# Kernel optimization log

Measured on AMD Instinct MI355X. Metric: run time of the kernel, lower is better.

The kernel has to match this reference:

```python
import jax, jax.numpy as jnp
import numpy as np

TOP_K = 2
NUM_EXPERTS = 64
LOAD_BALANCE_ALPHA = 0.01
Z_LOSS_ALPHA = 1e-4
TEMPERATURE = 1.0  # buffer init, clamped to [0.1, 2.0] -> 1.0 (seq_len < 8192 branch)


def setup_inputs() -> dict:
    key = jax.random.key(0)
    k1, k2 = jax.random.split(key)
    x = jax.random.normal(k1, (4, 4096, 1024), dtype=jnp.float32)
    gate_w = jax.random.normal(k2, (NUM_EXPERTS, 1024), dtype=jnp.float32) * (1.0 / np.sqrt(1024))
    return {"x": x, "gate_w": gate_w}


def reference(x, gate_w):
    B, S, H = x.shape
    x_flat = x.reshape(-1, H)                      # [T, H], T = B*S
    logits = jnp.einsum('th,eh->te', x_flat, gate_w)  # [T, E]
    logits = logits / TEMPERATURE
    scores = jax.nn.softmax(logits, axis=-1)       # [T, E]
    # eval path: dynamic_top_k == top_k, no noise / capacity limitation
    top_scores, top_idx = jax.lax.top_k(scores, TOP_K)   # [T, K]
    top_scores = jax.nn.softmax(top_scores.astype(jnp.float32), axis=-1).astype(x.dtype)
    # load-balance loss: squared deviation of mean expert load from uniform
    expert_load = scores.mean(axis=0)              # [E]
    ideal = 1.0 / NUM_EXPERTS
    lb_loss = LOAD_BALANCE_ALPHA * NUM_EXPERTS * jnp.sum((expert_load - ideal) ** 2)
    # z-loss: mean squared logsumexp of gate logits
    z = jax.nn.logsumexp(logits, axis=-1)          # [T]
    z_loss = Z_LOSS_ALPHA * jnp.mean(z ** 2)
    total_loss = lb_loss + z_loss
    return top_scores, top_idx, total_loss
```

## Files before the change

### kernel.cpp

```cpp
#include <hip/hip_runtime.h>
#include <math.h>

#define T_TOK 16384
#define NEXP  64


__global__ void moe_prep(const float* __restrict__ gw, float* __restrict__ ws) {
    __shared__ float tile[64][65];
    const int b = blockIdx.x;
    const int tid = threadIdx.x;
    if (b == 0 && tid < 128) ws[tid] = 0.f;
#pragma unroll
    for (int it = 0; it < 16; ++it) {
        int idx = it * 256 + tid;
        int e = idx >> 6, kk = idx & 63;
        tile[e][kk] = gw[e * 1024 + b * 64 + kk];
    }
    __syncthreads();
#pragma unroll
    for (int it = 0; it < 16; ++it) {
        int idx = it * 256 + tid;
        int kk = idx >> 6, e = idx & 63;
        ws[128 + (b * 64 + kk) * 64 + e] = tile[e][kk];
    }
}

__launch_bounds__(1024, 4)
__global__ void moe_main(const float* __restrict__ x,
                         const float* __restrict__ wt,
                         float* __restrict__ acc_ws,
                         float* __restrict__ out) {
    __shared__ float xbuf[2][4096];
    __shared__ float sc[64][65];
    __shared__ float row_inv[64];
    __shared__ float colpart[16][64];
    __shared__ int   is_last;

    const int tid  = threadIdx.x;
    const int lane = tid & 63;
    const int wv   = tid >> 6;
    const int g     = __builtin_amdgcn_readfirstlane(wv & 3);
    const int h     = __builtin_amdgcn_readfirstlane(wv >> 2);
    const int khalf = __builtin_amdgcn_readfirstlane(h >> 1);
    const int cq    = __builtin_amdgcn_readfirstlane(h & 1);
    const int tok0 = blockIdx.x << 6;

    const int rr = tid >> 4;
    const int cg = tid & 15;
    const float* gbase = x + (((size_t)(tok0 + rr)) << 10) + (cg << 2);
    const int lo = (rr << 6) + ((cg ^ (rr & 15)) << 2);
    float* xb = &xbuf[0][0];

    float acc[16];
#pragma unroll
    for (int e = 0; e < 16; ++e) acc[e] = 0.f;

    float4 p0 = *(const float4*)(gbase);
    float4 p1 = *(const float4*)(gbase + 512);

    const int swz = lane & 15;
    const float* xrow = &xbuf[khalf][lane << 6];

#pragma unroll 1
    for (int s = 0; s < 8; ++s) {
        __syncthreads();
        *(float4*)(xb + lo)        = p0;
        *(float4*)(xb + lo + 4096) = p1;
        __syncthreads();
        if (s < 7) {
            const float* gs = gbase + ((s + 1) << 6);
            p0 = *(const float4*)(gs);
            p1 = *(const float4*)(gs + 512);
        }
        const float* wrow = wt + (((khalf << 9) + (s << 6)) << 6) + (g << 4);
#pragma unroll
        for (int c = 0; c < 8; ++c) {
            int cc = (cq << 3) + c;
            float4 xv = *(const float4*)(xrow + ((cc ^ swz) << 2));
            float xa[4] = {xv.x, xv.y, xv.z, xv.w};
#pragma unroll
            for (int j = 0; j < 4; ++j) {
                const float* wkj = wrow + (((cc << 2) + j) << 6);
                float xj = xa[j];
#pragma unroll
                for (int e = 0; e < 16; ++e)
                    acc[e] = fmaf(xj, wkj[e], acc[e]);
            }
        }
    }

    if (h == 0) {
#pragma unroll
        for (int e = 0; e < 16; ++e) sc[lane][(g << 4) + e] = acc[e];
    }
    __syncthreads();
    if (h == 1) {
#pragma unroll
        for (int e = 0; e < 16; ++e) sc[lane][(g << 4) + e] += acc[e];
    }
    __syncthreads();
    if (h == 2) {
#pragma unroll
        for (int e = 0; e < 16; ++e) sc[lane][(g << 4) + e] += acc[e];
    }
    __syncthreads();
    if (h == 3) {
#pragma unroll
        for (int e = 0; e < 16; ++e) sc[lane][(g << 4) + e] += acc[e];
    }
    __syncthreads();

    if (tid < 64) {
        const int r = tid;
        float v1 = -1e30f, v2 = -1e30f;
        int i1 = 0, i2 = 0;
        for (int j = 0; j < 64; ++j) {
            float l = sc[r][j];
            if (l > v1)      { v2 = v1; i2 = i1; v1 = l; i1 = j; }
            else if (l > v2) { v2 = l; i2 = j; }
        }
        float m = v1;
        float ssum = 0.f;
        for (int j = 0; j < 64; ++j) {
            float ev = expf(sc[r][j] - m);
            ssum += ev;
            sc[r][j] = ev;
        }
        float inv = 1.f / ssum;
        row_inv[r] = inv;
        float z = m + logf(ssum);
        float zsq = z * z;
#pragma unroll
        for (int off = 32; off > 0; off >>= 1) zsq += __shfl_down(zsq, off);
        if (lane == 0) atomicAdd(acc_ws + 64, zsq);

        float p1s = inv;
        float p2s = expf(v2 - m) * inv;
        float bb  = expf(p2s - p1s);
        float s1 = 1.f / (1.f + bb);
        float s2 = bb * s1;
        int t = tok0 + r;
        out[2 * t]     = s1;
        out[2 * t + 1] = s2;
        out[2 * T_TOK + 2 * t]     = (float)i1;
        out[2 * T_TOK + 2 * t + 1] = (float)i2;
    }
    __syncthreads();

    {
        int e  = tid & 63;
        int rg = tid >> 6;
        float sum = 0.f;
#pragma unroll
        for (int r2 = 0; r2 < 4; ++r2) {
            int row = (rg << 2) + r2;
            sum += sc[row][e] * row_inv[row];
        }
        colpart[rg][e] = sum;
    }
    __syncthreads();
    if (tid < 64) {
        float tot = 0.f;
#pragma unroll
        for (int rg = 0; rg < 16; ++rg) tot += colpart[rg][tid];
        atomicAdd(acc_ws + tid, tot);
    }

    __syncthreads();
    if (tid == 0) {
        __threadfence();
        int old = __hip_atomic_fetch_add((int*)(acc_ws + 66), 1,
                                         __ATOMIC_ACQ_REL, __HIP_MEMORY_SCOPE_AGENT);
        is_last = (old == 255) ? 1 : 0;
    }
    __syncthreads();
    if (is_last && tid < 64) {
        __threadfence();
        float load = __hip_atomic_load(acc_ws + tid, __ATOMIC_RELAXED,
                                       __HIP_MEMORY_SCOPE_AGENT) * (1.f / 16384.f);
        float d = load - (1.f / 64.f);
        float v = d * d;
#pragma unroll
        for (int off = 32; off > 0; off >>= 1) v += __shfl_down(v, off);
        if (tid == 0) {
            float zsum = __hip_atomic_load(acc_ws + 64, __ATOMIC_RELAXED,
                                           __HIP_MEMORY_SCOPE_AGENT);
            float lb = 0.01f * 64.f * v;
            float zl = 1e-4f * zsum * (1.f / 16384.f);
            out[4 * T_TOK] = lb + zl;
        }
    }
}

extern "C" void kernel_launch(void* const* d_in, const int* in_sizes, int n_in,
                              void* d_out, int out_size, void* d_ws, size_t ws_size,
                              hipStream_t stream) {
    const float* x  = (const float*)d_in[0];
    const float* gw = (const float*)d_in[1];
    float* out = (float*)d_out;
    float* ws  = (float*)d_ws;

    moe_prep<<<16, 256, 0, stream>>>(gw, ws);
    moe_main<<<256, 1024, 0, stream>>>(x, ws + 128, ws, out);
}
```

Before: 134.8 us.

## Stage gate weights in LDS and use 4x4 register tiles for logits

The inner GEMV loop now stages both an x tile and a weight tile in shared memory for each 64-wide K chunk. Each thread computes a 4-token by 4-expert register tile instead of one token against 16 experts read straight from global memory. This is meant to cut redundant global and L1 reads of the transposed weights and raise the FMA-to-load ratio through outer-product reuse. In exchange it runs twice as many pipeline stages and barriers (16 instead of 8), and the logit buffer is repadded to a row stride of 68 so the partial sums can be stored as float4.

```diff
diff --git a/kernel.cpp b/kernel.cpp
--- a/kernel.cpp
+++ b/kernel.cpp
@@ -30,8 +30,9 @@
                          const float* __restrict__ wt,
                          float* __restrict__ acc_ws,
                          float* __restrict__ out) {
-    __shared__ float xbuf[2][4096];
-    __shared__ float sc[64][65];
+    __shared__ float xbuf[4096];
+    __shared__ float wbuf[4096];
+    __shared__ float sc[64 * 68];
     __shared__ float row_inv[64];
     __shared__ float colpart[16][64];
     __shared__ int   is_last;
@@ -39,92 +40,136 @@
     const int tid  = threadIdx.x;
     const int lane = tid & 63;
     const int wv   = tid >> 6;
-    const int g     = __builtin_amdgcn_readfirstlane(wv & 3);
-    const int h     = __builtin_amdgcn_readfirstlane(wv >> 2);
-    const int khalf = __builtin_amdgcn_readfirstlane(h >> 1);
-    const int cq    = __builtin_amdgcn_readfirstlane(h & 1);
+    const int kq   = __builtin_amdgcn_readfirstlane(wv & 3);
+    const int tile = __builtin_amdgcn_readfirstlane(wv >> 2);
+    const int tt = tile >> 1, te = tile & 1;
+    const int ta = lane >> 3;
+    const int eb = lane & 7;
     const int tok0 = blockIdx.x << 6;
 
     const int rr = tid >> 4;
     const int cg = tid & 15;
-    const float* gbase = x + (((size_t)(tok0 + rr)) << 10) + (cg << 2);
-    const int lo = (rr << 6) + ((cg ^ (rr & 15)) << 2);
-    float* xb = &xbuf[0][0];
+    const float* gx = x + (((size_t)(tok0 + rr)) << 10) + ((cg >> 2) << 8) + ((cg & 3) << 2);
+    const int xlo = (rr << 6) + ((cg ^ (rr & 15)) << 2);
+    const float* gw = wt + ((((rr >> 4) << 8) + (rr & 15)) << 6) + (cg << 2);
+    const int wlo = (rr << 6) + (cg << 2);
 
     float acc[16];
 #pragma unroll
     for (int e = 0; e < 16; ++e) acc[e] = 0.f;
 
-    float4 p0 = *(const float4*)(gbase);
-    float4 p1 = *(const float4*)(gbase + 512);
-
-    const int swz = lane & 15;
-    const float* xrow = &xbuf[khalf][lane << 6];
+    const int t0 = (tt << 5) + (ta << 2);
+    const float* xrow0 = xbuf + ((t0 + 0) << 6);
+    const float* xrow1 = xbuf + ((t0 + 1) << 6);
+    const float* xrow2 = xbuf + ((t0 + 2) << 6);
+    const float* xrow3 = xbuf + ((t0 + 3) << 6);
+    const int c0 = (t0 + 0) & 15, c1 = (t0 + 1) & 15;
+    const int c2 = (t0 + 2) & 15, c3 = (t0 + 3) & 15;
+    const int ebase = (te << 5) + (eb << 2);
+    const float* wp = wbuf + (kq << 10) + ebase;
+    const int cwb = kq << 2;
+
+    float4 px = *(const float4*)gx;
+    float4 pw = *(const float4*)gw;
 
 #pragma unroll 1
-    for (int s = 0; s < 8; ++s) {
+    for (int s = 0; s < 16; ++s) {
         __syncthreads();
-        *(float4*)(xb + lo)        = p0;
-        *(float4*)(xb + lo + 4096) = p1;
+        *(float4*)(xbuf + xlo) = px;
+        *(float4*)(wbuf + wlo) = pw;
         __syncthreads();
-        if (s < 7) {
-            const float* gs = gbase + ((s + 1) << 6);
-            p0 = *(const float4*)(gs);
-            p1 = *(const float4*)(gs + 512);
-        }
-        const float* wrow = wt + (((khalf << 9) + (s << 6)) << 6) + (g << 4);
-#pragma unroll
-        for (int c = 0; c < 8; ++c) {
-            int cc = (cq << 3) + c;
-            float4 xv = *(const float4*)(xrow + ((cc ^ swz) << 2));
-            float xa[4] = {xv.x, xv.y, xv.z, xv.w};
-#pragma unroll
-            for (int j = 0; j < 4; ++j) {
-                const float* wkj = wrow + (((cc << 2) + j) << 6);
-                float xj = xa[j];
-#pragma unroll
-                for (int e = 0; e < 16; ++e)
-                    acc[e] = fmaf(xj, wkj[e], acc[e]);
-            }
-        }
-    }
-
-    if (h == 0) {
-#pragma unroll
-        for (int e = 0; e < 16; ++e) sc[lane][(g << 4) + e] = acc[e];
-    }
-    __syncthreads();
-    if (h == 1) {
-#pragma unroll
-        for (int e = 0; e < 16; ++e) sc[lane][(g << 4) + e] += acc[e];
-    }
-    __syncthreads();
-    if (h == 2) {
-#pragma unroll
-        for (int e = 0; e < 16; ++e) sc[lane][(g << 4) + e] += acc[e];
-    }
-    __syncthreads();
-    if (h == 3) {
-#pragma unroll
-        for (int e = 0; e < 16; ++e) sc[lane][(g << 4) + e] += acc[e];
+        if (s < 15) {
+            px = *(const float4*)(gx + ((s + 1) << 4));
+            pw = *(const float4*)(gw + ((s + 1) << 10));
+        }
+#pragma unroll
+        for (int g4 = 0; g4 < 4; ++g4) {
+            const int cw = cwb + g4;
+            float4 xf0 = *(const float4*)(xrow0 + ((cw ^ c0) << 2));
+            float4 xf1 = *(const float4*)(xrow1 + ((cw ^ c1) << 2));
+            float4 xf2 = *(const float4*)(xrow2 + ((cw ^ c2) << 2));
+            float4 xf3 = *(const float4*)(xrow3 + ((cw ^ c3) << 2));
+            const float* wq = wp + (g4 << 8);
+            float4 wf0 = *(const float4*)(wq);
+            float4 wf1 = *(const float4*)(wq + 64);
+            float4 wf2 = *(const float4*)(wq + 128);
+            float4 wf3 = *(const float4*)(wq + 192);
+            float xa[16] = {xf0.x, xf0.y, xf0.z, xf0.w,
+                            xf1.x, xf1.y, xf1.z, xf1.w,
+                            xf2.x, xf2.y, xf2.z, xf2.w,
+                            xf3.x, xf3.y, xf3.z, xf3.w};
+            float wa[16] = {wf0.x, wf0.y, wf0.z, wf0.w,
+                            wf1.x, wf1.y, wf1.z, wf1.w,
+                            wf2.x, wf2.y, wf2.z, wf2.w,
+                            wf3.x, wf3.y, wf3.z, wf3.w};
+#pragma unroll
+            for (int i = 0; i < 4; ++i)
+#pragma unroll
+                for (int u = 0; u < 4; ++u) {
+                    float xv = xa[(i << 2) + u];
+#pragma unroll
+                    for (int j = 0; j < 4; ++j)
+                        acc[(i << 2) + j] = fmaf(xv, wa[(u << 2) + j], acc[(i << 2) + j]);
+                }
+        }
+    }
+
+    if (kq == 0) {
+#pragma unroll
+        for (int i = 0; i < 4; ++i) {
+            float4 v = make_float4(acc[(i << 2)], acc[(i << 2) + 1],
+                                   acc[(i << 2) + 2], acc[(i << 2) + 3]);
+            *(float4*)(sc + (t0 + i) * 68 + ebase) = v;
+        }
+    }
+    __syncthreads();
+    if (kq == 1) {
+#pragma unroll
+        for (int i = 0; i < 4; ++i) {
+            float4 o = *(float4*)(sc + (t0 + i) * 68 + ebase);
+            o.x += acc[(i << 2)];     o.y += acc[(i << 2) + 1];
+            o.z += acc[(i << 2) + 2]; o.w += acc[(i << 2) + 3];
+            *(float4*)(sc + (t0 + i) * 68 + ebase) = o;
+        }
+    }
+    __syncthreads();
+    if (kq == 2) {
+#pragma unroll
+        for (int i = 0; i < 4; ++i) {
+            float4 o = *(float4*)(sc + (t0 + i) * 68 + ebase);
+            o.x += acc[(i << 2)];     o.y += acc[(i << 2) + 1];
+            o.z += acc[(i << 2) + 2]; o.w += acc[(i << 2) + 3];
+            *(float4*)(sc + (t0 + i) * 68 + ebase) = o;
+        }
+    }
+    __syncthreads();
+    if (kq == 3) {
+#pragma unroll
+        for (int i = 0; i < 4; ++i) {
+            float4 o = *(float4*)(sc + (t0 + i) * 68 + ebase);
+            o.x += acc[(i << 2)];     o.y += acc[(i << 2) + 1];
+            o.z += acc[(i << 2) + 2]; o.w += acc[(i << 2) + 3];
+            *(float4*)(sc + (t0 + i) * 68 + ebase) = o;
+        }
     }
     __syncthreads();
 
     if (tid < 64) {
         const int r = tid;
+        const float* srow = sc + r * 68;
         float v1 = -1e30f, v2 = -1e30f;
         int i1 = 0, i2 = 0;
         for (int j = 0; j < 64; ++j) {
-            float l = sc[r][j];
+            float l = srow[j];
             if (l > v1)      { v2 = v1; i2 = i1; v1 = l; i1 = j; }
             else if (l > v2) { v2 = l; i2 = j; }
         }
         float m = v1;
         float ssum = 0.f;
         for (int j = 0; j < 64; ++j) {
-            float ev = expf(sc[r][j] - m);
+            float ev = expf(srow[j] - m);
             ssum += ev;
-            sc[r][j] = ev;
+            sc[r * 68 + j] = ev;
         }
         float inv = 1.f / ssum;
         row_inv[r] = inv;
@@ -154,7 +199,7 @@
 #pragma unroll
         for (int r2 = 0; r2 < 4; ++r2) {
             int row = (rg << 2) + r2;
-            sum += sc[row][e] * row_inv[row];
+            sum += sc[row * 68 + e] * row_inv[row];
         }
         colpart[rg][e] = sum;
     }
```

Result: faster. 130.6 us (-3.1%).

## Stage gate weights in LDS and use 8x8 register-tiled outer-product GEMM

Applied to the files above, without the earlier changes.

Replaces the pre-transposed global weight read with per-block LDS staging of both x and gate_w tiles (padded stride 68). Each thread now computes an 8-token by 8-expert outer-product tile with 64 accumulators, and the 16 waves split the K dimension. The separate transpose kernel is dropped for a trivial zeroing kernel. The cost is a longer serialized cross-wave reduction through LDS in eight sync-separated rounds, plus higher register pressure under the 1024-thread launch bound.

```diff
diff --git a/kernel.cpp b/kernel.cpp
--- a/kernel.cpp
+++ b/kernel.cpp
@@ -3,35 +3,32 @@
 
 #define T_TOK 16384
 #define NEXP  64
-
-
-__global__ void moe_prep(const float* __restrict__ gw, float* __restrict__ ws) {
-    __shared__ float tile[64][65];
-    const int b = blockIdx.x;
-    const int tid = threadIdx.x;
-    if (b == 0 && tid < 128) ws[tid] = 0.f;
-#pragma unroll
-    for (int it = 0; it < 16; ++it) {
-        int idx = it * 256 + tid;
-        int e = idx >> 6, kk = idx & 63;
-        tile[e][kk] = gw[e * 1024 + b * 64 + kk];
-    }
-    __syncthreads();
-#pragma unroll
-    for (int it = 0; it < 16; ++it) {
-        int idx = it * 256 + tid;
-        int kk = idx >> 6, e = idx & 63;
-        ws[128 + (b * 64 + kk) * 64 + e] = tile[e][kk];
-    }
+#define STR   68
+
+
+__global__ void moe_zero(float* __restrict__ ws) {
+    if (threadIdx.x < 128) ws[threadIdx.x] = 0.f;
 }
+
+#define FMA_ROW(i, xv) do {                                                    \
+    acc[((i) << 3) + 0] = fmaf((xv), wf0.x, acc[((i) << 3) + 0]);              \
+    acc[((i) << 3) + 1] = fmaf((xv), wf0.y, acc[((i) << 3) + 1]);              \
+    acc[((i) << 3) + 2] = fmaf((xv), wf0.z, acc[((i) << 3) + 2]);              \
+    acc[((i) << 3) + 3] = fmaf((xv), wf0.w, acc[((i) << 3) + 3]);              \
+    acc[((i) << 3) + 4] = fmaf((xv), wf1.x, acc[((i) << 3) + 4]);              \
+    acc[((i) << 3) + 5] = fmaf((xv), wf1.y, acc[((i) << 3) + 5]);              \
+    acc[((i) << 3) + 6] = fmaf((xv), wf1.z, acc[((i) << 3) + 6]);              \
+    acc[((i) << 3) + 7] = fmaf((xv), wf1.w, acc[((i) << 3) + 7]);              \
+} while (0)
 
 __launch_bounds__(1024, 4)
 __global__ void moe_main(const float* __restrict__ x,
-                         const float* __restrict__ wt,
+                         const float* __restrict__ gw,
                          float* __restrict__ acc_ws,
                          float* __restrict__ out) {
-    __shared__ float xbuf[2][4096];
-    __shared__ float sc[64][65];
+    __shared__ __align__(16) float xbuf[64 * STR];
+    __shared__ __align__(16) float wbuf[64 * STR];
+    __shared__ __align__(16) float sc[64 * STR];
     __shared__ float row_inv[64];
     __shared__ float colpart[16][64];
     __shared__ int   is_last;
@@ -39,92 +36,125 @@
     const int tid  = threadIdx.x;
     const int lane = tid & 63;
     const int wv   = tid >> 6;
-    const int g     = __builtin_amdgcn_readfirstlane(wv & 3);
-    const int h     = __builtin_amdgcn_readfirstlane(wv >> 2);
-    const int khalf = __builtin_amdgcn_readfirstlane(h >> 1);
-    const int cq    = __builtin_amdgcn_readfirstlane(h & 1);
+    const int kbase = __builtin_amdgcn_readfirstlane(wv << 2);
+    const int tq = lane >> 3;
+    const int eq = lane & 7;
     const int tok0 = blockIdx.x << 6;
 
-    const int rr = tid >> 4;
-    const int cg = tid & 15;
-    const float* gbase = x + (((size_t)(tok0 + rr)) << 10) + (cg << 2);
-    const int lo = (rr << 6) + ((cg ^ (rr & 15)) << 2);
-    float* xb = &xbuf[0][0];
-
-    float acc[16];
-#pragma unroll
-    for (int e = 0; e < 16; ++e) acc[e] = 0.f;
-
-    float4 p0 = *(const float4*)(gbase);
-    float4 p1 = *(const float4*)(gbase + 512);
-
-    const int swz = lane & 15;
-    const float* xrow = &xbuf[khalf][lane << 6];
+    const int srow = tid >> 4;
+    const int kc   = tid & 15;
+    const float* gx = x  + ((size_t)(tok0 + srow) << 10) + kc;
+    const float* gwp = gw + ((size_t)srow << 10) + kc;
+    const int slo = kc * STR + srow;
+
+    float acc[64];
+#pragma unroll
+    for (int i = 0; i < 64; ++i) acc[i] = 0.f;
+
+    float px0 = gx[0],  px1 = gx[16],  px2 = gx[32],  px3 = gx[48];
+    float pw0 = gwp[0], pw1 = gwp[16], pw2 = gwp[32], pw3 = gwp[48];
+
+    const float* xr = xbuf + kbase * STR + (tq << 3);
+    const float* wr = wbuf + kbase * STR + (eq << 3);
 
 #pragma unroll 1
-    for (int s = 0; s < 8; ++s) {
+    for (int s = 0; s < 16; ++s) {
         __syncthreads();
-        *(float4*)(xb + lo)        = p0;
-        *(float4*)(xb + lo + 4096) = p1;
+        xbuf[slo]            = px0;
+        xbuf[slo + 16 * STR] = px1;
+        xbuf[slo + 32 * STR] = px2;
+        xbuf[slo + 48 * STR] = px3;
+        wbuf[slo]            = pw0;
+        wbuf[slo + 16 * STR] = pw1;
+        wbuf[slo + 32 * STR] = pw2;
+        wbuf[slo + 48 * STR] = pw3;
         __syncthreads();
-        if (s < 7) {
-            const float* gs = gbase + ((s + 1) << 6);
-            p0 = *(const float4*)(gs);
-            p1 = *(const float4*)(gs + 512);
-        }
-        const float* wrow = wt + (((khalf << 9) + (s << 6)) << 6) + (g << 4);
-#pragma unroll
-        for (int c = 0; c < 8; ++c) {
-            int cc = (cq << 3) + c;
-            float4 xv = *(const float4*)(xrow + ((cc ^ swz) << 2));
-            float xa[4] = {xv.x, xv.y, xv.z, xv.w};
-#pragma unroll
-            for (int j = 0; j < 4; ++j) {
-                const float* wkj = wrow + (((cc << 2) + j) << 6);
-                float xj = xa[j];
-#pragma unroll
-                for (int e = 0; e < 16; ++e)
-                    acc[e] = fmaf(xj, wkj[e], acc[e]);
+        if (s < 15) {
+            const float* g2 = gx  + ((s + 1) << 6);
+            const float* g3 = gwp + ((s + 1) << 6);
+            px0 = g2[0]; px1 = g2[16]; px2 = g2[32]; px3 = g2[48];
+            pw0 = g3[0]; pw1 = g3[16]; pw2 = g3[32]; pw3 = g3[48];
+        }
+#pragma unroll
+        for (int kk = 0; kk < 4; ++kk) {
+            float4 xf0 = *(const float4*)(xr + kk * STR);
+            float4 xf1 = *(const float4*)(xr + kk * STR + 4);
+            float4 wf0 = *(const float4*)(wr + kk * STR);
+            float4 wf1 = *(const float4*)(wr + kk * STR + 4);
+            FMA_ROW(0, xf0.x); FMA_ROW(1, xf0.y);
+            FMA_ROW(2, xf0.z); FMA_ROW(3, xf0.w);
+            FMA_ROW(4, xf1.x); FMA_ROW(5, xf1.y);
+            FMA_ROW(6, xf1.z); FMA_ROW(7, xf1.w);
+        }
+    }
+
+    __syncthreads();
+#pragma unroll 1
+    for (int c = 0; c < 8; ++c) {
+        if (wv == c) {
+#pragma unroll
+            for (int i = 0; i < 8; ++i) {
+                float* p = sc + ((tq << 3) + i) * STR + (eq << 3);
+                float4 a0 = make_float4(acc[(i << 3) + 0], acc[(i << 3) + 1],
+                                        acc[(i << 3) + 2], acc[(i << 3) + 3]);
+                float4 a1 = make_float4(acc[(i << 3) + 4], acc[(i << 3) + 5],
+                                        acc[(i << 3) + 6], acc[(i << 3) + 7]);
+                if (c == 0) {
+                    *(float4*)p = a0; *(float4*)(p + 4) = a1;
+                } else {
+                    float4 o0 = *(float4*)p, o1 = *(float4*)(p + 4);
+                    o0.x += a0.x; o0.y += a0.y; o0.z += a0.z; o0.w += a0.w;
+                    o1.x += a1.x; o1.y += a1.y; o1.z += a1.z; o1.w += a1.w;
+                    *(float4*)p = o0; *(float4*)(p + 4) = o1;
+                }
             }
-        }
-    }
-
-    if (h == 0) {
-#pragma unroll
-        for (int e = 0; e < 16; ++e) sc[lane][(g << 4) + e] = acc[e];
-    }
-    __syncthreads();
-    if (h == 1) {
-#pragma unroll
-        for (int e = 0; e < 16; ++e) sc[lane][(g << 4) + e] += acc[e];
-    }
-    __syncthreads();
-    if (h == 2) {
-#pragma unroll
-        for (int e = 0; e < 16; ++e) sc[lane][(g << 4) + e] += acc[e];
-    }
-    __syncthreads();
-    if (h == 3) {
-#pragma unroll
-        for (int e = 0; e < 16; ++e) sc[lane][(g << 4) + e] += acc[e];
+        } else if (wv == 8 + c) {
+#pragma unroll
+            for (int i = 0; i < 8; ++i) {
+                float* p = xbuf + ((tq << 3) + i) * STR + (eq << 3);
+                float4 a0 = make_float4(acc[(i << 3) + 0], acc[(i << 3) + 1],
+                                        acc[(i << 3) + 2], acc[(i << 3) + 3]);
+                float4 a1 = make_float4(acc[(i << 3) + 4], acc[(i << 3) + 5],
+                                        acc[(i << 3) + 6], acc[(i << 3) + 7]);
+                if (c == 0) {
+                    *(float4*)p = a0; *(float4*)(p + 4) = a1;
+                } else {
+                    float4 o0 = *(float4*)p, o1 = *(float4*)(p + 4);
+                    o0.x += a0.x; o0.y += a0.y; o0.z += a0.z; o0.w += a0.w;
+                    o1.x += a1.x; o1.y += a1.y; o1.z += a1.z; o1.w += a1.w;
+                    *(float4*)p = o0; *(float4*)(p + 4) = o1;
+                }
+            }
+        }
+        __syncthreads();
+    }
+    {
+        float4* s4 = (float4*)sc;
+        const float4* b4 = (const float4*)xbuf;
+        for (int i = tid; i < (64 * STR) / 4; i += 1024) {
+            float4 a = s4[i], b = b4[i];
+            a.x += b.x; a.y += b.y; a.z += b.z; a.w += b.w;
+            s4[i] = a;
+        }
     }
     __syncthreads();
 
     if (tid < 64) {
         const int r = tid;
+        const float* srow2 = sc + r * STR;
         float v1 = -1e30f, v2 = -1e30f;
         int i1 = 0, i2 = 0;
         for (int j = 0; j < 64; ++j) {
-            float l = sc[r][j];
+            float l = srow2[j];
             if (l > v1)      { v2 = v1; i2 = i1; v1 = l; i1 = j; }
             else if (l > v2) { v2 = l; i2 = j; }
         }
         float m = v1;
         float ssum = 0.f;
         for (int j = 0; j < 64; ++j) {
-            float ev = expf(sc[r][j] - m);
+            float ev = expf(srow2[j] - m);
             ssum += ev;
-            sc[r][j] = ev;
+            sc[r * STR + j] = ev;
         }
         float inv = 1.f / ssum;
         row_inv[r] = inv;
@@ -154,7 +184,7 @@
 #pragma unroll
         for (int r2 = 0; r2 < 4; ++r2) {
             int row = (rg << 2) + r2;
-            sum += sc[row][e] * row_inv[row];
+            sum += sc[row * STR + e] * row_inv[row];
         }
         colpart[rg][e] = sum;
     }
@@ -200,6 +230,6 @@
     float* out = (float*)d_out;
     float* ws  = (float*)d_ws;
 
-    moe_prep<<<16, 256, 0, stream>>>(gw, ws);
-    moe_main<<<256, 1024, 0, stream>>>(x, ws + 128, ws, out);
+    moe_zero<<<1, 128, 0, stream>>>(ws);
+    moe_main<<<256, 1024, 0, stream>>>(x, gw, ws, out);
 }
```

New measurement: 133.1 us. Within noise of the previous version (-1.2%).
